# Optimization experiments

Hardware: AMD Instinct MI355X
Metric: run time of the kernel (lower is better)

## Reference

```python
import jax, jax.numpy as jnp
import numpy as np

N, F, H = 100000, 128, 2
DH = F // H  # per-head dim = 64
E = 1600000


def setup_inputs() -> dict:
    key = jax.random.key(0)
    ks = jax.random.split(key, 10)
    s = 0.05
    return {
        "nodes": jax.random.normal(ks[0], (N, F), jnp.float32),
        "edge_index": jax.random.randint(ks[1], (2, E), 0, N, jnp.int64),
        # TransformerConv linear layers (stored as [in, out] so we do x @ W)
        "Wq": jax.random.normal(ks[2], (F, F), jnp.float32) * s,
        "bq": jnp.zeros((F,), jnp.float32),
        "Wk": jax.random.normal(ks[3], (F, F), jnp.float32) * s,
        "bk": jnp.zeros((F,), jnp.float32),
        "Wv": jax.random.normal(ks[4], (F, F), jnp.float32) * s,
        "bv": jnp.zeros((F,), jnp.float32),
        "Wskip": jax.random.normal(ks[5], (F, F), jnp.float32) * s,
        "bskip": jnp.zeros((F,), jnp.float32),
        # gate: Linear(2F, F, bias=False); fuse: Linear(F, F, bias=False)
        "Wgate": jax.random.normal(ks[6], (2 * F, F), jnp.float32) * s,
        "Wfuse": jax.random.normal(ks[7], (F, F), jnp.float32) * s,
    }


def transformer_conv(nodes, src, dst, Wq, bq, Wk, bk, Wv, bv, Wskip, bskip):
    n = nodes.shape[0]
    q = (nodes @ Wq + bq).reshape(n, H, DH)
    k = (nodes @ Wk + bk).reshape(n, H, DH)
    v = (nodes @ Wv + bv).reshape(n, H, DH)
    # per-edge attention logits: [E, H]
    alpha = jnp.einsum("ehd,ehd->eh", q[dst], k[src]) / jnp.sqrt(jnp.float32(DH))
    # segment softmax over incoming edges of each destination node
    amax = jax.ops.segment_max(alpha, dst, num_segments=n)  # [N, H]
    ex = jnp.exp(alpha - amax[dst])
    denom = jax.ops.segment_sum(ex, dst, num_segments=n)  # [N, H]
    w = ex / denom[dst]  # [E, H]
    msg = v[src] * w[:, :, None]  # [E, H, DH]
    agg = jax.ops.segment_sum(msg, dst, num_segments=n).reshape(n, F)
    # root/skip connection (beta=0 -> plain add)
    return agg + nodes @ Wskip + bskip


def reference(nodes, edge_index, Wq, bq, Wk, bk, Wv, bv, Wskip, bskip, Wgate, Wfuse):
    src, dst = edge_index[0], edge_index[1]
    x = transformer_conv(nodes, src, dst, Wq, bq, Wk, bk, Wv, bv, Wskip, bskip)
    h = jnp.concatenate([nodes, x], axis=-1)  # [N, 2F]
    gate = jax.nn.sigmoid(h @ Wgate)  # [N, F]
    fuse = jnp.tanh(x @ Wfuse)  # [N, F]
    return gate * fuse + (1.0 - gate) * nodes
```

## Files before the change

kernel.cpp:

```cpp
#include <hip/hip_runtime.h>
#include <hip/hip_fp8.h>
#include <stdint.h>

#define NN 100000
#define EE 1600000
#define FF 128
#define CAP 60

typedef __attribute__((ext_vector_type(8)))  short bf16x8;
typedef __attribute__((ext_vector_type(8)))  unsigned short u16x8;
typedef __attribute__((ext_vector_type(2)))  float f32x2;
typedef __attribute__((ext_vector_type(16))) float f32x16;

#define NB_BLOCKS    6250
#define PREP_BLOCKS  450
#define CNT0_BLOCKS  98
#define BUILD2_BLOCKS 1563
#define QKVS_BLOCKS  12500
#define F2_BLOCKS    (BUILD2_BLOCKS + QKVS_BLOCKS)

#define QSCALE 0.1803368801111244f

__device__ __forceinline__ float bf2f(unsigned short u) {
    union { unsigned int i; float f; } c; c.i = ((unsigned int)u) << 16; return c.f;
}
__device__ __forceinline__ unsigned short f2bf(float f) {
    union { unsigned int i; float f; } c; c.f = f;
    unsigned int u = c.i;
    return (unsigned short)((u + 0x7FFFu + ((u >> 16) & 1u)) >> 16);
}
__device__ __forceinline__ float fp82f(unsigned int b) {
    __hip_fp8_e4m3 t; t.__x = (__hip_fp8_storage_t)(b & 0xFFu); return (float)t;
}
__device__ __forceinline__ unsigned char f2fp8(float f) {
    __hip_fp8_e4m3 t(f); return (unsigned char)t.__x;
}
template<bool HI>
__device__ __forceinline__ f32x2 cvtpk8(unsigned int w) {
#if __has_builtin(__builtin_amdgcn_cvt_pk_f32_fp8)
    return __builtin_amdgcn_cvt_pk_f32_fp8((int)w, HI);
#else
    f32x2 r;
    r[0] = fp82f(HI ? (w >> 16) : w);
    r[1] = fp82f(HI ? (w >> 24) : (w >> 8));
    return r;
#endif
}
__device__ __forceinline__ bf16x8 pack8(const float* p) {
    float4 f0 = *(const float4*)p;
    float4 f1 = *(const float4*)(p + 4);
    bf16x8 r;
    r[0] = (short)f2bf(f0.x); r[1] = (short)f2bf(f0.y);
    r[2] = (short)f2bf(f0.z); r[3] = (short)f2bf(f0.w);
    r[4] = (short)f2bf(f1.x); r[5] = (short)f2bf(f1.y);
    r[6] = (short)f2bf(f1.z); r[7] = (short)f2bf(f1.w);
    return r;
}

__global__ __launch_bounds__(256) void k_f1(
    const float* __restrict__ nodes, unsigned short* __restrict__ nb,
    const float* __restrict__ Wq, const float* __restrict__ Wk,
    const float* __restrict__ Wv, const float* __restrict__ Ws,
    const float* __restrict__ Wg, const float* __restrict__ Wf,
    const float* __restrict__ bq, const float* __restrict__ bk,
    const float* __restrict__ bv, const float* __restrict__ bs,
    unsigned short* __restrict__ Wp, unsigned short* __restrict__ Wp2,
    float* __restrict__ bias, int* __restrict__ count)
{
    const int bid = blockIdx.x;
    if (bid < NB_BLOCKS) {
        size_t i = ((size_t)bid * 256 + threadIdx.x) * 8;
        *(bf16x8*)(nb + i) = pack8(nodes + i);
    } else if (bid < NB_BLOCKS + PREP_BLOCKS) {
        int idx = (bid - NB_BLOCKS) * 256 + threadIdx.x;
        if (idx < 65536) {
            int j = idx & 7, lane = (idx >> 3) & 63, ks = (idx >> 9) & 7;
            int cf = (idx >> 12) & 3, cg = idx >> 14;
            int c  = cf * 32 + (lane & 31);
            int kk = ks * 16 + (lane >> 5) * 8 + j;
            const float* W = (cg == 0) ? Wq : (cg == 1) ? Wk : (cg == 2) ? Wv : Ws;
            Wp[idx] = f2bf(W[kk * FF + c]);
        } else if (idx < 65536 + 49152) {
            int p = idx - 65536;
            int j = p & 7, lane = (p >> 3) & 63, ks = (p >> 9) & 7;
            int cf = (p >> 12) & 3, mat = p >> 14;
            int c  = cf * 32 + (lane & 31);
            int kk = ks * 16 + (lane >> 5) * 8 + j;
            float v = (mat == 0) ? Wg[kk * FF + c]
                    : (mat == 1) ? Wg[(FF + kk) * FF + c]
                                 : Wf[kk * FF + c];
            Wp2[p] = f2bf(v);
        } else if (idx < 65536 + 49152 + 512) {
            int j = idx - (65536 + 49152);
            float b = (j < 128) ? bq[j] : (j < 256) ? bk[j - 128]
                    : (j < 384) ? bv[j - 256] : bs[j - 384];
            bias[j] = b;
        }
    } else {
        int j = ((bid - NB_BLOCKS - PREP_BLOCKS) * 256 + threadIdx.x) * 4;
        if (j < NN) *(int4*)(count + j) = make_int4(0, 0, 0, 0);
    }
}

__global__ __launch_bounds__(256) void k_f2(
    const int* __restrict__ src, const int* __restrict__ dst,
    int* __restrict__ count, int* __restrict__ srclist,
    const unsigned short* __restrict__ nb, const unsigned short* __restrict__ Wp,
    const float* __restrict__ bias, unsigned short* __restrict__ qb,
    unsigned char* __restrict__ kvb, unsigned short* __restrict__ skb)
{
    const int bid = blockIdx.x;
    if (bid % 9 == 0) {
        const int bb = bid / 9;
        const int e0 = bb * 1024 + threadIdx.x;
        #pragma unroll
        for (int j = 0; j < 4; ++j) {
            const int e = e0 + j * 256;
            if (e < EE) {
                int d = __builtin_nontemporal_load(&dst[e]);
                int s = __builtin_nontemporal_load(&src[e]);
                int r = atomicAdd(&count[d], 1);
                if (r < CAP) __builtin_nontemporal_store(s, &srclist[(size_t)d * CAP + r]);
            }
        }
        return;
    }
    const int q = bid - bid / 9 - 1;
    const int row0 = (q >> 2) * 32;
    const int cg = q & 3;
    const int wave = threadIdx.x >> 6, lane = threadIdx.x & 63;
    const int arow = row0 + (lane & 31);
    const int khalf = lane >> 5;
    const int cf = wave;

    f32x16 acc;
    #pragma unroll
    for (int r = 0; r < 16; ++r) acc[r] = 0.f;

    const unsigned short* ap = nb + (size_t)arow * FF + khalf * 8;
    #pragma unroll
    for (int ks = 0; ks < 8; ++ks) {
        bf16x8 a = *(const bf16x8*)(ap + ks * 16);
        bf16x8 b = *(const bf16x8*)(Wp + (((cg * 4 + cf) * 8 + ks) << 9) + (lane << 3));
        acc = __builtin_amdgcn_mfma_f32_32x32x16_bf16(a, b, acc, 0, 0, 0);
    }

    const int col = cf * 32 + (lane & 31);
    const float bv = bias[cg * 128 + col];
    #pragma unroll
    for (int r = 0; r < 16; ++r) {
        const int rr = row0 + (r & 3) + 8 * (r >> 2) + 4 * (lane >> 5);
        const float fv = acc[r] + bv;
        if (cg == 0)      qb [(size_t)rr * 128 + col] = f2bf(fv);
        else if (cg == 1) kvb[(size_t)rr * 256 + (col >> 2) * 8 + (col & 3)]     = f2fp8(fv);
        else if (cg == 2) kvb[(size_t)rr * 256 + (col >> 2) * 8 + 4 + (col & 3)] = f2fp8(fv);
        else              skb[(size_t)rr * 128 + col] = f2bf(fv);
    }
}

__global__ __launch_bounds__(256, 4) void k_f3(
    const unsigned short* __restrict__ nb, const unsigned short* __restrict__ qb,
    const unsigned char* __restrict__ kvb, const unsigned short* __restrict__ skb,
    const unsigned short* __restrict__ Wp2,
    const int* __restrict__ count, const int* __restrict__ srclist,
    float* __restrict__ out)
{
    __shared__ unsigned short xl[32 * 128];
    const int wave = threadIdx.x >> 6, lane = threadIdx.x & 63;
    const int row0 = blockIdx.x * 32;

    const int es = lane >> 4;
    const int le = lane & 15;
    const int slane = lane < CAP ? lane : CAP - 1;

    {
        const int wid0 = row0 + wave * 8;
    }
    int   deg_n  = count[row0 + wave * 8];
    u16x8 qr_n   = *(const u16x8*)(qb  + (size_t)(row0 + wave * 8) * FF + le * 8);
    int   sreg_n = srclist[(size_t)(row0 + wave * 8) * CAP + slane];
    u16x8 sr_n   = *(const u16x8*)(skb + (size_t)(row0 + wave * 8) * FF + le * 8);

    #pragma unroll 1
    for (int i = 0; i < 8; ++i) {
        const int rl  = wave * 8 + i;
        const int wid = row0 + rl;

        int deg = __builtin_amdgcn_readfirstlane(deg_n);
        if (deg > CAP) deg = CAP;
        const u16x8 qr  = qr_n;
        const int   sreg = sreg_n;
        const u16x8 sr  = sr_n;

        if (i < 7) {
            const int widn = wid + 1;
            deg_n  = count[widn];
            qr_n   = *(const u16x8*)(qb  + (size_t)widn * FF + le * 8);
            sreg_n = srclist[(size_t)widn * CAP + slane];
            sr_n   = *(const u16x8*)(skb + (size_t)widn * FF + le * 8);
        }

        f32x2 qa0, qa1, qa2, qa3;
        qa0[0] = bf2f(qr[0]) * QSCALE; qa0[1] = bf2f(qr[1]) * QSCALE;
        qa1[0] = bf2f(qr[2]) * QSCALE; qa1[1] = bf2f(qr[3]) * QSCALE;
        qa2[0] = bf2f(qr[4]) * QSCALE; qa2[1] = bf2f(qr[5]) * QSCALE;
        qa3[0] = bf2f(qr[6]) * QSCALE; qa3[1] = bf2f(qr[7]) * QSCALE;

        float denom = 0.f;
        f32x2 a01 = {0.f, 0.f}, a23 = {0.f, 0.f}, a45 = {0.f, 0.f}, a67 = {0.f, 0.f};

        const int nit = (deg + 3) >> 2;
        #pragma unroll 4
        for (int it = 0; it < nit; ++it) {
            const int idx  = 4 * it + es;
            const int sidx = idx < deg ? idx : deg - 1;
            const int s    = __shfl(sreg, sidx);
            const uint4 kv = *(const uint4*)(kvb + (size_t)s * 256 + le * 16);
            f32x2 pp = qa0 * cvtpk8<false>(kv.x);
            pp += qa1 * cvtpk8<true>(kv.x);
            pp += qa2 * cvtpk8<false>(kv.z);
            pp += qa3 * cvtpk8<true>(kv.z);
            float p = pp[0] + pp[1];
            p += __shfl_xor(p, 1);
            p += __shfl_xor(p, 2);
            p += __shfl_xor(p, 4);
            const float ex = (idx < deg) ? exp2f(p) : 0.f;
            denom += ex;
            f32x2 exv; exv[0] = ex; exv[1] = ex;
            a01 += exv * cvtpk8<false>(kv.y);
            a23 += exv * cvtpk8<true>(kv.y);
            a45 += exv * cvtpk8<false>(kv.w);
            a67 += exv * cvtpk8<true>(kv.w);
        }
        denom += __shfl_xor(denom, 16);
        denom += __shfl_xor(denom, 32);
        float af[8] = {a01[0], a01[1], a23[0], a23[1], a45[0], a45[1], a67[0], a67[1]};
        #pragma unroll
        for (int j = 0; j < 8; ++j) {
            af[j] += __shfl_xor(af[j], 16);
            af[j] += __shfl_xor(af[j], 32);
        }

        if (es == 0) {
            const float inv = (denom > 0.f) ? (1.0f / denom) : 0.f;
            u16x8 o;
            #pragma unroll
            for (int j = 0; j < 8; ++j) o[j] = f2bf(fmaf(af[j], inv, bf2f(sr[j])));
            *(u16x8*)&xl[rl * 128 + ((le ^ (rl & 7)) << 3)] = o;
        }
    }
    __syncthreads();

    const int arow = row0 + (lane & 31);
    const int khalf = lane >> 5;
    const int cf = wave;

    f32x16 gacc, facc;
    #pragma unroll
    for (int r = 0; r < 16; ++r) { gacc[r] = 0.f; facc[r] = 0.f; }

    #pragma unroll
    for (int ks = 0; ks < 8; ++ks) {
        bf16x8 an = *(const bf16x8*)(nb + (size_t)arow * FF + ks * 16 + khalf * 8);
        const int g2 = ks * 2 + khalf;
        bf16x8 ax = *(const bf16x8*)&xl[(lane & 31) * 128 + ((g2 ^ ((lane & 31) & 7)) << 3)];
        bf16x8 b0 = *(const bf16x8*)(Wp2 + (((0 * 4 + cf) * 8 + ks) << 9) + (lane << 3));
        bf16x8 b1 = *(const bf16x8*)(Wp2 + (((1 * 4 + cf) * 8 + ks) << 9) + (lane << 3));
        bf16x8 b2 = *(const bf16x8*)(Wp2 + (((2 * 4 + cf) * 8 + ks) << 9) + (lane << 3));
        gacc = __builtin_amdgcn_mfma_f32_32x32x16_bf16(an, b0, gacc, 0, 0, 0);
        gacc = __builtin_amdgcn_mfma_f32_32x32x16_bf16(ax, b1, gacc, 0, 0, 0);
        facc = __builtin_amdgcn_mfma_f32_32x32x16_bf16(ax, b2, facc, 0, 0, 0);
    }

    const int col = cf * 32 + (lane & 31);
    #pragma unroll
    for (int r = 0; r < 16; ++r) {
        const int rr = row0 + (r & 3) + 8 * (r >> 2) + 4 * (lane >> 5);
        const float g  = 1.0f / (1.0f + __expf(-gacc[r]));
        const float e2 = __expf(2.0f * facc[r]);
        const float fv = (e2 - 1.0f) / (e2 + 1.0f);
        const float nv = bf2f(nb[(size_t)rr * FF + col]);
        out[(size_t)rr * FF + col] = g * fv + (1.0f - g) * nv;
    }
}

extern "C" void kernel_launch(void* const* d_in, const int* in_sizes, int n_in,
                              void* d_out, int out_size, void* d_ws, size_t ws_size,
                              hipStream_t stream) {
    const float* nodes = (const float*)d_in[0];
    const int*   ei    = (const int*)d_in[1];
    const int*   esrc  = ei;
    const int*   edst  = ei + EE;
    const float* Wq = (const float*)d_in[2];
    const float* bq = (const float*)d_in[3];
    const float* Wk = (const float*)d_in[4];
    const float* bk = (const float*)d_in[5];
    const float* Wv = (const float*)d_in[6];
    const float* bv = (const float*)d_in[7];
    const float* Ws = (const float*)d_in[8];
    const float* bs = (const float*)d_in[9];
    const float* Wg = (const float*)d_in[10];
    const float* Wf = (const float*)d_in[11];
    float* out = (float*)d_out;

    char* wsb = (char*)d_ws;
    unsigned short* qb   = (unsigned short*)wsb;
    unsigned char*  kvb  = (unsigned char*)(qb + (size_t)NN * 128);
    unsigned short* skb  = (unsigned short*)(kvb + (size_t)NN * 256);
    unsigned short* nb   = skb + (size_t)NN * 128;
    unsigned short* Wp   = nb + (size_t)NN * 128;
    unsigned short* Wp2  = Wp + 65536;
    float* bias  = (float*)(Wp2 + 49152);
    int* count   = (int*)(bias + 512);
    int* srclist = count + NN;

    k_f1<<<NB_BLOCKS + PREP_BLOCKS + CNT0_BLOCKS, 256, 0, stream>>>(
        nodes, nb, Wq, Wk, Wv, Ws, Wg, Wf, bq, bk, bv, bs, Wp, Wp2, bias, count);
    k_f2<<<F2_BLOCKS, 256, 0, stream>>>(
        esrc, edst, count, srclist, nb, Wp, bias, qb, kvb, skb);
    k_f3<<<NN / 32, 256, 0, stream>>>(
        nb, qb, kvb, skb, Wp2, count, srclist, out);
}
```

Before: 249.3 us.

## Bucket edges by destination block before CSR build, drop bf16 node copy

Replaces the per-edge global atomic scatter into the adjacency list with a two-phase scheme. Edges are first binned into coarse destination buckets using shared-memory staging and batched global atomics, then a new kernel builds per-node counts and source lists with shared-memory atomics per bucket. It also removes the separate fp32-to-bf16 node conversion pass and converts on the fly in the GEMM kernels. This trades scattered global atomics and an extra node-sized write for an extra launch, a pair-buffer round trip, and fixed bucket capacities that could silently drop edges under skewed inputs.

```diff
diff --git a/kernel.cpp b/kernel.cpp
--- a/kernel.cpp
+++ b/kernel.cpp
@@ -6,18 +6,20 @@
 #define EE 1600000
 #define FF 128
 #define CAP 60
+#define NBKT 196
+#define BCAP 12288
+#define LBCAP 16
 
 typedef __attribute__((ext_vector_type(8)))  short bf16x8;
 typedef __attribute__((ext_vector_type(8)))  unsigned short u16x8;
 typedef __attribute__((ext_vector_type(2)))  float f32x2;
 typedef __attribute__((ext_vector_type(16))) float f32x16;
 
-#define NB_BLOCKS    6250
 #define PREP_BLOCKS  450
-#define CNT0_BLOCKS  98
-#define BUILD2_BLOCKS 1563
+#define F1_BLOCKS    (PREP_BLOCKS + 1)
+#define PH1_BLOCKS   196
 #define QKVS_BLOCKS  12500
-#define F2_BLOCKS    (BUILD2_BLOCKS + QKVS_BLOCKS)
+#define F2_BLOCKS    (QKVS_BLOCKS + PH1_BLOCKS)
 
 #define QSCALE 0.1803368801111244f
 
@@ -58,21 +60,17 @@
 }
 
 __global__ __launch_bounds__(256) void k_f1(
-    const float* __restrict__ nodes, unsigned short* __restrict__ nb,
     const float* __restrict__ Wq, const float* __restrict__ Wk,
     const float* __restrict__ Wv, const float* __restrict__ Ws,
     const float* __restrict__ Wg, const float* __restrict__ Wf,
     const float* __restrict__ bq, const float* __restrict__ bk,
     const float* __restrict__ bv, const float* __restrict__ bs,
     unsigned short* __restrict__ Wp, unsigned short* __restrict__ Wp2,
-    float* __restrict__ bias, int* __restrict__ count)
+    float* __restrict__ bias, int* __restrict__ gcur)
 {
     const int bid = blockIdx.x;
-    if (bid < NB_BLOCKS) {
-        size_t i = ((size_t)bid * 256 + threadIdx.x) * 8;
-        *(bf16x8*)(nb + i) = pack8(nodes + i);
-    } else if (bid < NB_BLOCKS + PREP_BLOCKS) {
-        int idx = (bid - NB_BLOCKS) * 256 + threadIdx.x;
+    if (bid < PREP_BLOCKS) {
+        int idx = bid * 256 + threadIdx.x;
         if (idx < 65536) {
             int j = idx & 7, lane = (idx >> 3) & 63, ks = (idx >> 9) & 7;
             int cf = (idx >> 12) & 3, cg = idx >> 14;
@@ -97,35 +95,60 @@
             bias[j] = b;
         }
     } else {
-        int j = ((bid - NB_BLOCKS - PREP_BLOCKS) * 256 + threadIdx.x) * 4;
-        if (j < NN) *(int4*)(count + j) = make_int4(0, 0, 0, 0);
+        if (threadIdx.x < 256) gcur[threadIdx.x] = 0;
     }
 }
 
 __global__ __launch_bounds__(256) void k_f2(
     const int* __restrict__ src, const int* __restrict__ dst,
-    int* __restrict__ count, int* __restrict__ srclist,
-    const unsigned short* __restrict__ nb, const unsigned short* __restrict__ Wp,
+    int* __restrict__ gcur, uint2* __restrict__ gbuf,
+    const float* __restrict__ nodes, const unsigned short* __restrict__ Wp,
     const float* __restrict__ bias, unsigned short* __restrict__ qb,
     unsigned char* __restrict__ kvb, unsigned short* __restrict__ skb)
 {
+    __shared__ int   lcur[NBKT];
+    __shared__ uint2 lbuf[NBKT][LBCAP];
     const int bid = blockIdx.x;
-    if (bid % 9 == 0) {
-        const int bb = bid / 9;
-        const int e0 = bb * 1024 + threadIdx.x;
-        #pragma unroll
-        for (int j = 0; j < 4; ++j) {
-            const int e = e0 + j * 256;
-            if (e < EE) {
-                int d = __builtin_nontemporal_load(&dst[e]);
-                int s = __builtin_nontemporal_load(&src[e]);
-                int r = atomicAdd(&count[d], 1);
-                if (r < CAP) __builtin_nontemporal_store(s, &srclist[(size_t)d * CAP + r]);
+    const bool isph1 = ((bid & 63) == 0) && ((bid >> 6) < PH1_BLOCKS);
+    if (isph1) {
+        const int pb = bid >> 6;
+        const int e0 = pb * 8192;
+        for (int b = threadIdx.x; b < NBKT; b += 256) lcur[b] = 0;
+        __syncthreads();
+        #pragma unroll 1
+        for (int ch = 0; ch < 4; ++ch) {
+            #pragma unroll
+            for (int u = 0; u < 8; ++u) {
+                const int e = e0 + ch * 2048 + u * 256 + threadIdx.x;
+                if (e < EE) {
+                    const int d = dst[e];
+                    const int s = src[e];
+                    const int b = d >> 9;
+                    const int pos = atomicAdd(&lcur[b], 1);
+                    if (pos < LBCAP) {
+                        lbuf[b][pos] = make_uint2((unsigned)d, (unsigned)s);
+                    } else {
+                        const int g = atomicAdd(&gcur[b], 1);
+                        if (g < BCAP) gbuf[(size_t)b * BCAP + g] = make_uint2((unsigned)d, (unsigned)s);
+                    }
+                }
             }
+            __syncthreads();
+            for (int b = threadIdx.x; b < NBKT; b += 256) {
+                int n = lcur[b]; if (n > LBCAP) n = LBCAP;
+                if (n > 0) {
+                    const int g = atomicAdd(&gcur[b], n);
+                    for (int t = 0; t < n; ++t)
+                        if (g + t < BCAP) gbuf[(size_t)b * BCAP + g + t] = lbuf[b][t];
+                }
+                lcur[b] = 0;
+            }
+            __syncthreads();
         }
         return;
     }
-    const int q = bid - bid / 9 - 1;
+    const int nph1b = bid / 64 + 1;
+    const int q = bid - (nph1b < PH1_BLOCKS ? nph1b : PH1_BLOCKS);
     const int row0 = (q >> 2) * 32;
     const int cg = q & 3;
     const int wave = threadIdx.x >> 6, lane = threadIdx.x & 63;
@@ -137,10 +160,10 @@
     #pragma unroll
     for (int r = 0; r < 16; ++r) acc[r] = 0.f;
 
-    const unsigned short* ap = nb + (size_t)arow * FF + khalf * 8;
+    const float* ap = nodes + (size_t)arow * FF + khalf * 8;
     #pragma unroll
     for (int ks = 0; ks < 8; ++ks) {
-        bf16x8 a = *(const bf16x8*)(ap + ks * 16);
+        bf16x8 a = pack8(ap + ks * 16);
         bf16x8 b = *(const bf16x8*)(Wp + (((cg * 4 + cf) * 8 + ks) << 9) + (lane << 3));
         acc = __builtin_amdgcn_mfma_f32_32x32x16_bf16(a, b, acc, 0, 0, 0);
     }
@@ -158,8 +181,30 @@
     }
 }
 
+__global__ __launch_bounds__(256) void k_f3b(
+    const uint2* __restrict__ gbuf, const int* __restrict__ gcur,
+    int* __restrict__ count, int* __restrict__ srclist)
+{
+    __shared__ int lcnt[512];
+    const int b = blockIdx.x;
+    for (int t = threadIdx.x; t < 512; t += 256) lcnt[t] = 0;
+    __syncthreads();
+    int n = gcur[b]; if (n > BCAP) n = BCAP;
+    const int d0 = b << 9;
+    for (int i = threadIdx.x; i < n; i += 256) {
+        const uint2 p = gbuf[(size_t)b * BCAP + i];
+        const int r = atomicAdd(&lcnt[(int)p.x - d0], 1);
+        if (r < CAP) srclist[(size_t)p.x * CAP + r] = (int)p.y;
+    }
+    __syncthreads();
+    for (int t = threadIdx.x; t < 512; t += 256) {
+        const int d = d0 + t;
+        if (d < NN) count[d] = lcnt[t];
+    }
+}
+
 __global__ __launch_bounds__(256, 4) void k_f3(
-    const unsigned short* __restrict__ nb, const unsigned short* __restrict__ qb,
+    const float* __restrict__ nodes, const unsigned short* __restrict__ qb,
     const unsigned char* __restrict__ kvb, const unsigned short* __restrict__ skb,
     const unsigned short* __restrict__ Wp2,
     const int* __restrict__ count, const int* __restrict__ srclist,
@@ -173,9 +218,6 @@
     const int le = lane & 15;
     const int slane = lane < CAP ? lane : CAP - 1;
 
-    {
-        const int wid0 = row0 + wave * 8;
-    }
     int   deg_n  = count[row0 + wave * 8];
     u16x8 qr_n   = *(const u16x8*)(qb  + (size_t)(row0 + wave * 8) * FF + le * 8);
     int   sreg_n = srclist[(size_t)(row0 + wave * 8) * CAP + slane];
@@ -261,7 +303,7 @@
 
     #pragma unroll
     for (int ks = 0; ks < 8; ++ks) {
-        bf16x8 an = *(const bf16x8*)(nb + (size_t)arow * FF + ks * 16 + khalf * 8);
+        bf16x8 an = pack8(nodes + (size_t)arow * FF + ks * 16 + khalf * 8);
         const int g2 = ks * 2 + khalf;
         bf16x8 ax = *(const bf16x8*)&xl[(lane & 31) * 128 + ((g2 ^ ((lane & 31) & 7)) << 3)];
         bf16x8 b0 = *(const bf16x8*)(Wp2 + (((0 * 4 + cf) * 8 + ks) << 9) + (lane << 3));
@@ -279,7 +321,7 @@
         const float g  = 1.0f / (1.0f + __expf(-gacc[r]));
         const float e2 = __expf(2.0f * facc[r]);
         const float fv = (e2 - 1.0f) / (e2 + 1.0f);
-        const float nv = bf2f(nb[(size_t)rr * FF + col]);
+        const float nv = nodes[(size_t)rr * FF + col];
         out[(size_t)rr * FF + col] = g * fv + (1.0f - g) * nv;
     }
 }
@@ -307,17 +349,19 @@
     unsigned short* qb   = (unsigned short*)wsb;
     unsigned char*  kvb  = (unsigned char*)(qb + (size_t)NN * 128);
     unsigned short* skb  = (unsigned short*)(kvb + (size_t)NN * 256);
-    unsigned short* nb   = skb + (size_t)NN * 128;
-    unsigned short* Wp   = nb + (size_t)NN * 128;
+    unsigned short* Wp   = skb + (size_t)NN * 128;
     unsigned short* Wp2  = Wp + 65536;
-    float* bias  = (float*)(Wp2 + 49152);
-    int* count   = (int*)(bias + 512);
-    int* srclist = count + NN;
-
-    k_f1<<<NB_BLOCKS + PREP_BLOCKS + CNT0_BLOCKS, 256, 0, stream>>>(
-        nodes, nb, Wq, Wk, Wv, Ws, Wg, Wf, bq, bk, bv, bs, Wp, Wp2, bias, count);
+    float* bias   = (float*)(Wp2 + 49152);
+    int* count    = (int*)(bias + 512);
+    int* srclist  = count + NN;
+    int* gcur     = srclist + (size_t)NN * CAP;
+    uint2* gbuf   = (uint2*)(gcur + 256);
+
+    k_f1<<<F1_BLOCKS, 256, 0, stream>>>(
+        Wq, Wk, Wv, Ws, Wg, Wf, bq, bk, bv, bs, Wp, Wp2, bias, gcur);
     k_f2<<<F2_BLOCKS, 256, 0, stream>>>(
-        esrc, edst, count, srclist, nb, Wp, bias, qb, kvb, skb);
+        esrc, edst, gcur, gbuf, nodes, Wp, bias, qb, kvb, skb);
+    k_f3b<<<NBKT, 256, 0, stream>>>(gbuf, gcur, count, srclist);
     k_f3<<<NN / 32, 256, 0, stream>>>(
-        nb, qb, kvb, skb, Wp2, count, srclist, out);
-}
+        nodes, qb, kvb, skb, Wp2, count, srclist, out);
+}
```

After: 441.6 us. +77.1%, slower.
